# Performance work log

Hardware: AMD Instinct MI355X
Metric: run time of the kernel (lower is better)

Reference implementation:

```python
import jax, jax.numpy as jnp
import numpy as np

N, M, FIN, FOUT, E = 8, 50000, 32, 32, 800000


def setup_inputs() -> dict:
    key = jax.random.key(0)
    ks = jax.random.split(key, 6)
    x = jax.random.normal(ks[0], (N, M, FIN), dtype=jnp.float32)
    adj_rows = jax.random.randint(ks[1], (E,), 0, M, dtype=jnp.int32)
    adj_cols = jax.random.randint(ks[2], (E,), 0, M, dtype=jnp.int32)
    adj_vals = jax.random.uniform(ks[3], (E,), dtype=jnp.float32)
    stdv = 1.0 / np.sqrt(FOUT)
    weight = jax.random.uniform(ks[4], (FIN, FOUT), dtype=jnp.float32, minval=-stdv, maxval=stdv)
    bias = jax.random.uniform(ks[5], (FOUT,), dtype=jnp.float32, minval=-stdv, maxval=stdv)
    return {"x": x, "adj_rows": adj_rows, "adj_cols": adj_cols,
            "adj_vals": adj_vals, "weight": weight, "bias": bias}


def reference(x, adj_rows, adj_cols, adj_vals, weight, bias):
    # spmm(adj, x) over the node axis M for every batch element.
    # adj is COO: out[:, r, :] += v * x[:, c, :] for each edge (r, c, v).
    xe = jnp.take(x, adj_cols, axis=1) * adj_vals[None, :, None]  # [N, E, Fin]
    y = jnp.zeros_like(x).at[:, adj_rows, :].add(xe)              # [N, M, Fin]
    # dense linear + bias: (N*M, Fin) @ (Fin, Fout) + bias
    return jnp.einsum('nmf,fo->nmo', y, weight) + bias
```

## Files before the change

kernel.cpp:

```cpp
#include <hip/hip_runtime.h>
#include <hip/hip_bf16.h>

#define NB 8
#define MN 50000
#define FI 32
#define FO 32
#define NE 800000
#define CAP 64
#define BINSHIFT 7
#define BINROWS 128
#define NBINS 391
#define BINCAPLOG 12
#define BIN_BLOCKS 98

typedef float        f32x4 __attribute__((ext_vector_type(4)));
typedef unsigned int u32x4 __attribute__((ext_vector_type(4)));

__global__ __launch_bounds__(256) void gemm_xw(const float* __restrict__ x,
                                               const float* __restrict__ W,
                                               unsigned int* __restrict__ zb,
                                               int* __restrict__ gCursor) {
    int bid = blockIdx.x;
    int t   = threadIdx.x;

    if (bid == 0) {
        for (int i = t; i < NBINS; i += 256) gCursor[i] = i << BINCAPLOG;
    }

    __shared__ float Ws[FI * FO];
    ((float4*)Ws)[t] = ((const float4*)W)[t];
    __syncthreads();

    int n     = bid / 3125;
    int mb    = bid % 3125;
    int rowid = t >> 4;
    int j     = t & 15;
    int m     = mb * 16 + rowid;

    const float4* xr = (const float4*)(x + ((long)n * MN + m) * FI);
    float4 xv[8];
#pragma unroll
    for (int i = 0; i < 8; ++i) xv[i] = xr[i];
    const float* xf = (const float*)xv;

    float a0 = 0.f, a1 = 0.f;
#pragma unroll
    for (int k = 0; k < FI; ++k) {
        a0 += xf[k] * Ws[k * FO + 2 * j];
        a1 += xf[k] * Ws[k * FO + 2 * j + 1];
    }
    unsigned int lo = (unsigned int)__bfloat16_as_ushort(__float2bfloat16(a0));
    unsigned int hi = (unsigned int)__bfloat16_as_ushort(__float2bfloat16(a1));
    zb[(long)m * 128 + n * 16 + j] = lo | (hi << 16);
}

__global__ __launch_bounds__(1024) void bin_edges(const int* __restrict__ rows,
                                                  const int* __restrict__ cols,
                                                  const float* __restrict__ vals,
                                                  int* __restrict__ gCursor,
                                                  unsigned long long* __restrict__ sorted) {
    __shared__ int cnt[NBINS];
    __shared__ int base[NBINS];
    int t = threadIdx.x;
    for (int i = t; i < NBINS; i += 1024) cnt[i] = 0;
    __syncthreads();

    unsigned long long pk[8];
    int bn[8], rk[8];
    int e0 = blockIdx.x * 8192;
#pragma unroll
    for (int k = 0; k < 8; ++k) {
        int e = e0 + k * 1024 + t;
        bn[k] = -1;
        if (e < NE) {
            int r = rows[e];
            unsigned int vb = (unsigned int)__bfloat16_as_ushort(__float2bfloat16(vals[e]));
            pk[k] = ((unsigned long long)(unsigned int)r << 32) |
                    (unsigned long long)((vb << 16) | (unsigned int)cols[e]);
            bn[k] = r >> BINSHIFT;
            rk[k] = atomicAdd(&cnt[bn[k]], 1);
        }
    }
    __syncthreads();
    for (int i = t; i < NBINS; i += 1024) base[i] = atomicAdd(&gCursor[i], cnt[i]);
    __syncthreads();
#pragma unroll
    for (int k = 0; k < 8; ++k) {
        if (bn[k] >= 0) {
            int pos = base[bn[k]] + rk[k];
            if (pos < ((bn[k] + 1) << BINCAPLOG))
                sorted[pos] = pk[k];
        }
    }
}

__global__ __launch_bounds__(1024) void fill_sorted(const unsigned long long* __restrict__ sorted,
                                                    const int* __restrict__ gCursor,
                                                    unsigned int* __restrict__ dense,
                                                    int* __restrict__ posCnt) {
    __shared__ int cntS[BINROWS];
    __shared__ int pfx[BINROWS];
    __shared__ int exS[BINROWS];
    int t   = threadIdx.x;
    int bin = blockIdx.x;
    if (t < BINROWS) cntS[t] = 0;
    __syncthreads();

    int beg = bin << BINCAPLOG;
    int n = gCursor[bin] - beg;
    if (n > (1 << BINCAPLOG)) n = 1 << BINCAPLOG;

    unsigned long long pk[4];
    int lr[4], sl[4];
#pragma unroll
    for (int k = 0; k < 4; ++k) {
        int i = t + k * 1024;
        lr[k] = -1;
        if (i < n) {
            pk[k] = __builtin_nontemporal_load(&sorted[beg + i]);
            lr[k] = ((int)(pk[k] >> 32)) & (BINROWS - 1);
            sl[k] = atomicAdd(&cntS[lr[k]], 1);
        }
    }
    __syncthreads();

    if (t < BINROWS) pfx[t] = cntS[t] > CAP ? CAP : cntS[t];
    __syncthreads();
    for (int off = 1; off < BINROWS; off <<= 1) {
        int v = (t < BINROWS && t >= off) ? pfx[t - off] : 0;
        __syncthreads();
        if (t < BINROWS) pfx[t] += v;
        __syncthreads();
    }
    if (t < BINROWS) {
        int cc = cntS[t] > CAP ? CAP : cntS[t];
        exS[t] = pfx[t] - cc;
        int R = (bin << BINSHIFT) + t;
        if (R < MN) posCnt[R] = ((beg + exS[t]) << 7) | cc;
    }
    __syncthreads();

#pragma unroll
    for (int k = 0; k < 4; ++k) {
        if (lr[k] >= 0 && sl[k] < CAP)
            dense[beg + exS[lr[k]] + sl[k]] = (unsigned int)pk[k];
    }
}

__global__ __launch_bounds__(256) void aggregate(const u32x4* __restrict__ zb4,
                                                 const int* __restrict__ posCnt,
                                                 const unsigned int* __restrict__ dense,
                                                 const float* __restrict__ bias,
                                                 f32x4* __restrict__ out4) {
    int lane = threadIdx.x & 63;
    int r    = blockIdx.x * 4 + (threadIdx.x >> 6);

    int pc  = posCnt[r];
    int cnt = pc & 127;
    long pos = (unsigned int)pc >> 7;

    unsigned int mypk = __builtin_nontemporal_load(&dense[pos + lane]);

    int half = lane >> 5;
    int sub  = lane & 31;

    float acc[8];
#pragma unroll
    for (int k = 0; k < 8; ++k) acc[k] = 0.f;

    int i = 0;
    for (; i + 8 <= cnt; i += 8) {
        unsigned int pk[4];
        u32x4 zv[4];
#pragma unroll
        for (int k = 0; k < 4; ++k) pk[k] = __shfl(mypk, i + 2 * k + half);
#pragma unroll
        for (int k = 0; k < 4; ++k) zv[k] = zb4[((long)(pk[k] & 0xffff) << 5) + sub];
#pragma unroll
        for (int k = 0; k < 4; ++k) {
            float v = __uint_as_float(pk[k] & 0xffff0000u);
#pragma unroll
            for (int q = 0; q < 4; ++q) {
                unsigned int w = zv[k][q];
                acc[2 * q]     += v * __uint_as_float(w << 16);
                acc[2 * q + 1] += v * __uint_as_float(w & 0xffff0000u);
            }
        }
    }
    for (; i + 2 <= cnt; i += 2) {
        unsigned int pk0 = __shfl(mypk, i + half);
        u32x4 zv0 = zb4[((long)(pk0 & 0xffff) << 5) + sub];
        float v = __uint_as_float(pk0 & 0xffff0000u);
#pragma unroll
        for (int q = 0; q < 4; ++q) {
            unsigned int w = zv0[q];
            acc[2 * q]     += v * __uint_as_float(w << 16);
            acc[2 * q + 1] += v * __uint_as_float(w & 0xffff0000u);
        }
    }
    if (i < cnt) {
        unsigned int pk0 = __shfl(mypk, i);
        int   c = (half == 0) ? (int)(pk0 & 0xffff) : 0;
        float v = (half == 0) ? __uint_as_float(pk0 & 0xffff0000u) : 0.f;
        u32x4 zv0 = zb4[((long)c << 5) + sub];
#pragma unroll
        for (int q = 0; q < 4; ++q) {
            unsigned int w = zv0[q];
            acc[2 * q]     += v * __uint_as_float(w << 16);
            acc[2 * q + 1] += v * __uint_as_float(w & 0xffff0000u);
        }
    }

#pragma unroll
    for (int k = 0; k < 8; ++k) acc[k] += __shfl_xor(acc[k], 32);

    if (half == 0) {
        int n  = sub >> 2;
        int j4 = sub & 3;
        const float* bb = bias + j4 * 8;
        f32x4 o0 = {acc[0] + bb[0], acc[1] + bb[1], acc[2] + bb[2], acc[3] + bb[3]};
        f32x4 o1 = {acc[4] + bb[4], acc[5] + bb[5], acc[6] + bb[6], acc[7] + bb[7]};
        long ob = ((long)n * MN + r) * 8 + j4 * 2;
        __builtin_nontemporal_store(o0, &out4[ob]);
        __builtin_nontemporal_store(o1, &out4[ob + 1]);
    }
}

extern "C" void kernel_launch(void* const* d_in, const int* in_sizes, int n_in,
                              void* d_out, int out_size, void* d_ws, size_t ws_size,
                              hipStream_t stream) {
    const float* x    = (const float*)d_in[0];
    const int*   rows = (const int*)d_in[1];
    const int*   cols = (const int*)d_in[2];
    const float* vals = (const float*)d_in[3];
    const float* W    = (const float*)d_in[4];
    const float* bias = (const float*)d_in[5];
    f32x4* out4 = (f32x4*)d_out;

    char* ws = (char*)d_ws;
    size_t off_z      = 0;
    size_t off_pc     = off_z + (size_t)MN * NB * FO * 2;
    size_t off_gcur   = off_pc + (size_t)MN * 4;
    size_t off_dense  = off_gcur + (((size_t)NBINS * 4 + 127) & ~(size_t)127);
    size_t off_sorted = off_dense + (((size_t)NBINS << BINCAPLOG) + 64) * 4;

    unsigned int*       zb      = (unsigned int*)(ws + off_z);
    int*                posCnt  = (int*)(ws + off_pc);
    int*                gCursor = (int*)(ws + off_gcur);
    unsigned int*       dense   = (unsigned int*)(ws + off_dense);
    unsigned long long* sorted  = (unsigned long long*)(ws + off_sorted);

    gemm_xw<<<25000, 256, 0, stream>>>(x, W, zb, gCursor);

    bin_edges<<<BIN_BLOCKS, 1024, 0, stream>>>(rows, cols, vals, gCursor, sorted);

    fill_sorted<<<NBINS, 1024, 0, stream>>>(sorted, gCursor, dense, posCnt);

    aggregate<<<MN / 4, 256, 0, stream>>>((const u32x4*)zb, posCnt, dense, bias, out4);
}
```

Baseline: 115.5 us.

## Stage binned edges in shared memory for coalesced scatter and use more blocks

The bin_edges kernel now runs more, smaller blocks that each handle fewer edges. Each block runs an exclusive prefix scan over its bin counts, sorts its edges into bin order in shared memory, and then writes them out sequentially, so consecutive threads write consecutive addresses within each bin's global segment. The goal is to replace scattered 8-byte global writes with mostly contiguous runs and to spread the work over more CUs. In exchange it adds a shared-memory scan with several barriers and many more global atomics on gCursor, since each of the additional blocks does its own per-bin reservation.

```diff
diff --git a/kernel.cpp b/kernel.cpp
--- a/kernel.cpp
+++ b/kernel.cpp
@@ -11,7 +11,8 @@
 #define BINROWS 128
 #define NBINS 391
 #define BINCAPLOG 12
-#define BIN_BLOCKS 98
+#define BIN_BLOCKS 392
+#define BIN_EDGES_BLK 2048
 
 typedef float        f32x4 __attribute__((ext_vector_type(4)));
 typedef unsigned int u32x4 __attribute__((ext_vector_type(4)));
@@ -54,23 +55,25 @@
     zb[(long)m * 128 + n * 16 + j] = lo | (hi << 16);
 }
 
-__global__ __launch_bounds__(1024) void bin_edges(const int* __restrict__ rows,
-                                                  const int* __restrict__ cols,
-                                                  const float* __restrict__ vals,
-                                                  int* __restrict__ gCursor,
-                                                  unsigned long long* __restrict__ sorted) {
+__global__ __launch_bounds__(256) void bin_edges(const int* __restrict__ rows,
+                                                 const int* __restrict__ cols,
+                                                 const float* __restrict__ vals,
+                                                 int* __restrict__ gCursor,
+                                                 unsigned long long* __restrict__ sorted) {
     __shared__ int cnt[NBINS];
-    __shared__ int base[NBINS];
+    __shared__ int excl[NBINS];
+    __shared__ int gbase[NBINS];
+    __shared__ unsigned long long stage[BIN_EDGES_BLK];
     int t = threadIdx.x;
-    for (int i = t; i < NBINS; i += 1024) cnt[i] = 0;
+    for (int i = t; i < NBINS; i += 256) cnt[i] = 0;
     __syncthreads();
 
     unsigned long long pk[8];
     int bn[8], rk[8];
-    int e0 = blockIdx.x * 8192;
+    int e0 = blockIdx.x * BIN_EDGES_BLK;
 #pragma unroll
     for (int k = 0; k < 8; ++k) {
-        int e = e0 + k * 1024 + t;
+        int e = e0 + k * 256 + t;
         bn[k] = -1;
         if (e < NE) {
             int r = rows[e];
@@ -82,15 +85,40 @@
         }
     }
     __syncthreads();
-    for (int i = t; i < NBINS; i += 1024) base[i] = atomicAdd(&gCursor[i], cnt[i]);
-    __syncthreads();
+
+    for (int i = t; i < NBINS; i += 256) excl[i] = cnt[i];
+    __syncthreads();
+    for (int off = 1; off < NBINS; off <<= 1) {
+        int v0 = 0, v1 = 0;
+        int i0 = t, i1 = t + 256;
+        if (i0 < NBINS && i0 >= off) v0 = excl[i0 - off];
+        if (i1 < NBINS && i1 >= off) v1 = excl[i1 - off];
+        __syncthreads();
+        if (i0 < NBINS) excl[i0] += v0;
+        if (i1 < NBINS) excl[i1] += v1;
+        __syncthreads();
+    }
+    for (int i = t; i < NBINS; i += 256) {
+        int c = cnt[i];
+        excl[i] -= c;
+        gbase[i] = c > 0 ? atomicAdd(&gCursor[i], c) : 0;
+    }
+    __syncthreads();
+
 #pragma unroll
     for (int k = 0; k < 8; ++k) {
-        if (bn[k] >= 0) {
-            int pos = base[bn[k]] + rk[k];
-            if (pos < ((bn[k] + 1) << BINCAPLOG))
-                sorted[pos] = pk[k];
-        }
+        if (bn[k] >= 0) stage[excl[bn[k]] + rk[k]] = pk[k];
+    }
+    __syncthreads();
+
+    int total = NE - e0;
+    if (total > BIN_EDGES_BLK) total = BIN_EDGES_BLK;
+    for (int s = t; s < total; s += 256) {
+        unsigned long long p = stage[s];
+        int b   = ((int)(p >> 32)) >> BINSHIFT;
+        int dst = gbase[b] + (s - excl[b]);
+        if (dst < ((b + 1) << BINCAPLOG))
+            sorted[dst] = p;
     }
 }
 
@@ -252,7 +280,7 @@
 
     gemm_xw<<<25000, 256, 0, stream>>>(x, W, zb, gCursor);
 
-    bin_edges<<<BIN_BLOCKS, 1024, 0, stream>>>(rows, cols, vals, gCursor, sorted);
+    bin_edges<<<BIN_BLOCKS, 256, 0, stream>>>(rows, cols, vals, gCursor, sorted);
 
     fill_sorted<<<NBINS, 1024, 0, stream>>>(sorted, gCursor, dense, posCnt);
 
```

Measured after the change: 121.1 us. +4.8%, slower.
